# Kernel tuning notes

Measured on AMD Instinct MI355X. Metric: run time of the kernel, lower is better.

## Reference

```python
import jax, jax.numpy as jnp
import numpy as np

D, K = 128, 32
B, H, W = 32, 96, 96


def setup_inputs() -> dict:
    key = jax.random.key(0)
    k1, k2, k3 = jax.random.split(key, 3)
    X = jax.random.normal(k1, (B, D, H, W), dtype=jnp.float32)
    std1 = 1.0 / float(np.sqrt(K * D))
    codewords = jax.random.uniform(k2, (K, D), dtype=jnp.float32, minval=-std1, maxval=std1)
    scale = jax.random.uniform(k3, (K,), dtype=jnp.float32, minval=-1.0, maxval=0.0)
    return {"X": X, "codewords": codewords, "scale": scale}


def reference(X, codewords, scale):
    b, d = X.shape[0], X.shape[1]
    # [B, D, H, W] -> [B, N, D]
    Xf = X.reshape(b, d, -1).transpose(0, 2, 1)
    # scale_l2: SL[b,n,k] = scale_k^2 * ||x_bn - c_k||^2 (no (B,N,K,D) materialization)
    x2 = jnp.sum(Xf * Xf, axis=-1)                      # [B, N]
    c2 = jnp.sum(codewords * codewords, axis=-1)        # [K]
    xc = jnp.einsum('bnd,kd->bnk', Xf, codewords)       # [B, N, K]
    sl = (scale * scale)[None, None, :] * (x2[:, :, None] - 2.0 * xc + c2[None, None, :])
    A = jax.nn.softmax(sl, axis=2)                      # [B, N, K]
    # aggregate: E[b,k,d] = sum_n A[b,n,k] * (x[b,n,d] - c[k,d])
    E = jnp.einsum('bnk,bnd->bkd', A, Xf) - jnp.sum(A, axis=1)[:, :, None] * codewords[None, :, :]
    return E
```

## Files before the change

kernel.cpp:

```cpp
#include <hip/hip_runtime.h>

#define B_ 32
#define D_ 128
#define K_ 32
#define N_ 9216
#define NT 256
#define NS 64
#define XDN_S 72
#define AKN_S 72
#define X2S_S 68

typedef __bf16 bf16x8_t __attribute__((ext_vector_type(8)));
typedef float f32x4_t __attribute__((ext_vector_type(4)));

__device__ __forceinline__ unsigned short f2bf(float f) {
    unsigned u = __float_as_uint(f);
    u = (u + 0x7fffu + ((u >> 16) & 1u)) >> 16;
    return (unsigned short)u;
}
__device__ __forceinline__ unsigned f2bf_pk(float lo, float hi) {
    unsigned a = __float_as_uint(lo);
    a = (a + 0x7fffu + ((a >> 16) & 1u)) >> 16;
    unsigned b = __float_as_uint(hi);
    b = (b + 0x7fffu + ((b >> 16) & 1u)) & 0xffff0000u;
    return a | b;
}
__device__ __forceinline__ void bar_lds() {
    asm volatile("s_waitcnt lgkmcnt(0)\n\ts_barrier" ::: "memory");
}

__global__ __launch_bounds__(256, 3) void k_fused(
        const float* __restrict__ X, const float* __restrict__ cw,
        const float* __restrict__ scale, float* __restrict__ ws) {
    __shared__ __align__(16) unsigned short X_nd[NS * 128];
    __shared__ __align__(16) unsigned short X_dn[D_ * XDN_S];
    __shared__ __align__(16) unsigned short CWb[K_ * 128];
    __shared__ __align__(16) unsigned short Akn[K_ * AKN_S];
    __shared__ float x2s[16 * X2S_S];
    __shared__ float u_s[K_], w_s[K_];
    __shared__ float sAw[4 * 34];
    __shared__ float sA[K_];

    const int t = threadIdx.x;
    const int w = t >> 6;
    const int l = t & 63;
    const int lm = l & 15;
    const int lq = l >> 4;
    const int d8 = t >> 4;
    const int n4 = t & 15;
    const int b = blockIdx.x / 36;
    const int n0 = (blockIdx.x % 36) * NT;

    #pragma unroll
    for (int i = 0; i < 4; ++i) {
        int idx = t + 256 * i;
        int k = idx >> 5, d4 = idx & 31;
        float4 c = ((const float4*)cw)[idx];
        int phys = (d4 >> 1) ^ (k & 15);
        unsigned* p = (unsigned*)&CWb[k * 128 + phys * 8 + (d4 & 1) * 4];
        p[0] = f2bf_pk(c.x, c.y);
        p[1] = f2bf_pk(c.z, c.w);
    }
    if (t < 32) {
        float sc = scale[t];
        float s2 = sc * sc;
        const float4* cr = (const float4*)(cw + t * 128);
        float c2 = 0.f;
        #pragma unroll 8
        for (int i = 0; i < 32; ++i) {
            float4 v = cr[i];
            c2 += v.x * v.x + v.y * v.y + v.z * v.z + v.w * v.w;
        }
        u_s[t] = s2;
        w_s[t] = s2 * c2;
    }
    __syncthreads();
    const float u0 = u_s[lm], u1 = u_s[16 + lm];
    const float w0 = w_s[lm], w1 = w_s[16 + lm];

    f32x4_t acc2[2][2];
    #pragma unroll
    for (int a = 0; a < 2; ++a)
        #pragma unroll
        for (int c = 0; c < 2; ++c)
            acc2[a][c] = (f32x4_t){0.f, 0.f, 0.f, 0.f};
    float ps0 = 0.f, ps1 = 0.f;

    const float* Xg = X + ((size_t)b * D_ + d8 * 8) * N_ + n0 + n4 * 4;
    float4 v[8];
    #pragma unroll
    for (int j = 0; j < 8; ++j) v[j] = *(const float4*)(Xg + (size_t)j * N_);

    for (int s = 0; s < 4; ++s) {
        bar_lds();
        float4 vn[8];
        if (s < 3) {
            const float* Xg2 = Xg + (s + 1) * NS;
            #pragma unroll
            for (int j = 0; j < 8; ++j) vn[j] = *(const float4*)(Xg2 + (size_t)j * N_);
        }
        #pragma unroll
        for (int jn = 0; jn < 4; ++jn) {
            float a = 0.f;
            #pragma unroll
            for (int j = 0; j < 8; ++j) {
                float xv = (&v[j].x)[jn];
                a += xv * xv;
            }
            x2s[d8 * X2S_S + n4 * 4 + jn] = a;
        }
        #pragma unroll
        for (int j = 0; j < 8; ++j) {
            unsigned* p = (unsigned*)&X_dn[(d8 * 8 + j) * XDN_S + n4 * 4];
            p[0] = f2bf_pk(v[j].x, v[j].y);
            p[1] = f2bf_pk(v[j].z, v[j].w);
        }
        #pragma unroll
        for (int jn = 0; jn < 4; ++jn) {
            unsigned q[4];
            #pragma unroll
            for (int j2 = 0; j2 < 4; ++j2)
                q[j2] = f2bf_pk((&v[2 * j2].x)[jn], (&v[2 * j2 + 1].x)[jn]);
            int row = n4 * 4 + jn;
            *(uint4*)&X_nd[row * 128 + ((d8 ^ (row & 15)) * 8)] = *(const uint4*)q;
        }
        bar_lds();
        float x2row = 0.f;
        #pragma unroll
        for (int g = 0; g < 16; ++g) x2row += x2s[g * X2S_S + l];
        f32x4_t acc1[2];
        acc1[0] = (f32x4_t){0.f, 0.f, 0.f, 0.f};
        acc1[1] = (f32x4_t){0.f, 0.f, 0.f, 0.f};
        #pragma unroll
        for (int ks = 0; ks < 4; ++ks) {
            int g = (ks * 4 + lq) ^ lm;
            bf16x8_t a  = *(const bf16x8_t*)&X_nd[(w * 16 + lm) * 128 + g * 8];
            bf16x8_t b0 = *(const bf16x8_t*)&CWb[lm * 128 + g * 8];
            bf16x8_t b1 = *(const bf16x8_t*)&CWb[(16 + lm) * 128 + g * 8];
            acc1[0] = __builtin_amdgcn_mfma_f32_16x16x32_bf16(a, b0, acc1[0], 0, 0, 0);
            acc1[1] = __builtin_amdgcn_mfma_f32_16x16x32_bf16(a, b1, acc1[1], 0, 0, 0);
        }
        #pragma unroll
        for (int r = 0; r < 4; ++r) {
            int nl = w * 16 + lq * 4 + r;
            float x2v = __shfl(x2row, lq * 4 + r + w * 16 - w * 16);
            x2v = __shfl(x2row, lq * 4 + r);
            x2v = __shfl(x2row, nl);
            float sl0 = u0 * x2v + w0 - 2.f * u0 * acc1[0][r];
            float sl1 = u1 * x2v + w1 - 2.f * u1 * acc1[1][r];
            float m = fmaxf(sl0, sl1);
            m = fmaxf(m, __shfl_xor(m, 1));
            m = fmaxf(m, __shfl_xor(m, 2));
            m = fmaxf(m, __shfl_xor(m, 4));
            m = fmaxf(m, __shfl_xor(m, 8));
            float p0 = __expf(sl0 - m);
            float p1 = __expf(sl1 - m);
            float sum = p0 + p1;
            sum += __shfl_xor(sum, 1);
            sum += __shfl_xor(sum, 2);
            sum += __shfl_xor(sum, 4);
            sum += __shfl_xor(sum, 8);
            float inv = 1.f / sum;
            p0 *= inv; p1 *= inv;
            ps0 += p0; ps1 += p1;
            Akn[lm * AKN_S + nl] = f2bf(p0);
            Akn[(16 + lm) * AKN_S + nl] = f2bf(p1);
        }
        bar_lds();
        #pragma unroll
        for (int ks = 0; ks < 2; ++ks) {
            bf16x8_t xa0 = *(const bf16x8_t*)&X_dn[(w * 16 + lm) * XDN_S + ks * 32 + lq * 8];
            bf16x8_t xa1 = *(const bf16x8_t*)&X_dn[((w + 4) * 16 + lm) * XDN_S + ks * 32 + lq * 8];
            bf16x8_t pb0 = *(const bf16x8_t*)&Akn[lm * AKN_S + ks * 32 + lq * 8];
            bf16x8_t pb1 = *(const bf16x8_t*)&Akn[(16 + lm) * AKN_S + ks * 32 + lq * 8];
            acc2[0][0] = __builtin_amdgcn_mfma_f32_16x16x32_bf16(xa0, pb0, acc2[0][0], 0, 0, 0);
            acc2[0][1] = __builtin_amdgcn_mfma_f32_16x16x32_bf16(xa0, pb1, acc2[0][1], 0, 0, 0);
            acc2[1][0] = __builtin_amdgcn_mfma_f32_16x16x32_bf16(xa1, pb0, acc2[1][0], 0, 0, 0);
            acc2[1][1] = __builtin_amdgcn_mfma_f32_16x16x32_bf16(xa1, pb1, acc2[1][1], 0, 0, 0);
        }
        if (s < 3) {
            #pragma unroll
            for (int j = 0; j < 8; ++j) v[j] = vn[j];
        }
    }

    ps0 += __shfl_xor(ps0, 16); ps0 += __shfl_xor(ps0, 32);
    ps1 += __shfl_xor(ps1, 16); ps1 += __shfl_xor(ps1, 32);
    __syncthreads();
    if (l < 16) {
        sAw[w * 34 + l] = ps0;
        sAw[w * 34 + 16 + l] = ps1;
    }
    __syncthreads();
    if (t < 32) sA[t] = sAw[t] + sAw[34 + t] + sAw[68 + t] + sAw[102 + t];
    __syncthreads();

    float* pout = ws + (size_t)blockIdx.x * (K_ * D_);
    #pragma unroll
    for (int di = 0; di < 2; ++di) {
        #pragma unroll
        for (int kt = 0; kt < 2; ++kt) {
            const int d0 = (w + di * 4) * 16 + lq * 4;
            const int k  = kt * 16 + lm;
            float4 o;
            #pragma unroll
            for (int r = 0; r < 4; ++r)
                (&o.x)[r] = acc2[di][kt][r] - sA[k] * cw[k * 128 + d0 + r];
            *(float4*)&pout[k * 128 + d0] = o;
        }
    }
}

__global__ __launch_bounds__(256) void k_reduce(
        const float* __restrict__ ws, float* __restrict__ out) {
    int i = blockIdx.x * 256 + threadIdx.x;
    int b = i >> 10;
    int j = i & 1023;
    const float4* p = (const float4*)ws + (size_t)b * 36 * 1024 + j;
    float4 s = make_float4(0.f, 0.f, 0.f, 0.f);
    #pragma unroll
    for (int c = 0; c < 36; ++c) {
        float4 v = p[(size_t)c * 1024];
        s.x += v.x; s.y += v.y; s.z += v.z; s.w += v.w;
    }
    ((float4*)out)[i] = s;
}

extern "C" void kernel_launch(void* const* d_in, const int* in_sizes, int n_in,
                              void* d_out, int out_size, void* d_ws, size_t ws_size,
                              hipStream_t stream) {
    const float* X     = (const float*)d_in[0];
    const float* cw    = (const float*)d_in[1];
    const float* scale = (const float*)d_in[2];
    float* out = (float*)d_out;
    float* ws  = (float*)d_ws;

    k_fused <<<dim3(B_ * 36), dim3(256), 0, stream>>>(X, cw, scale, ws);
    k_reduce<<<dim3(128),     dim3(256), 0, stream>>>(ws, out);
}
```

Baseline: 226.2 us.

## Transpose first MFMA so softmax reduces in-lane, enlarge per-block chunk, use exp2

Swaps the operands of the first MFMA so each lane holds the 8 codeword logits of a single point. The softmax max and sum then reduce mostly within registers plus two cross-lane shuffles, instead of four-step butterflies repeated for every row. The log2(e) factor is folded into the scale so the exponential can use the native exp2 and rcp builtins. Each block now processes 384 points (6 stages) over 24 chunks, which cuts partial-sum traffic and the reduce kernel's work but leaves 768 blocks. The bf16 conversion uses the compiler cast, and the x2 partial store is vectorised.

```diff
diff --git a/kernel.cpp b/kernel.cpp
--- a/kernel.cpp
+++ b/kernel.cpp
@@ -4,26 +4,23 @@
 #define D_ 128
 #define K_ 32
 #define N_ 9216
-#define NT 256
+#define NT 384
+#define NCH 24
 #define NS 64
 #define XDN_S 72
 #define AKN_S 72
 #define X2S_S 68
+#define L2E 1.4426950408889634f
 
 typedef __bf16 bf16x8_t __attribute__((ext_vector_type(8)));
 typedef float f32x4_t __attribute__((ext_vector_type(4)));
 
 __device__ __forceinline__ unsigned short f2bf(float f) {
-    unsigned u = __float_as_uint(f);
-    u = (u + 0x7fffu + ((u >> 16) & 1u)) >> 16;
-    return (unsigned short)u;
+    return __builtin_bit_cast(unsigned short, (__bf16)f);
 }
 __device__ __forceinline__ unsigned f2bf_pk(float lo, float hi) {
-    unsigned a = __float_as_uint(lo);
-    a = (a + 0x7fffu + ((a >> 16) & 1u)) >> 16;
-    unsigned b = __float_as_uint(hi);
-    b = (b + 0x7fffu + ((b >> 16) & 1u)) & 0xffff0000u;
-    return a | b;
+    return (unsigned)__builtin_bit_cast(unsigned short, (__bf16)lo) |
+           ((unsigned)__builtin_bit_cast(unsigned short, (__bf16)hi) << 16);
 }
 __device__ __forceinline__ void bar_lds() {
     asm volatile("s_waitcnt lgkmcnt(0)\n\ts_barrier" ::: "memory");
@@ -48,8 +45,8 @@
     const int lq = l >> 4;
     const int d8 = t >> 4;
     const int n4 = t & 15;
-    const int b = blockIdx.x / 36;
-    const int n0 = (blockIdx.x % 36) * NT;
+    const int b = blockIdx.x / NCH;
+    const int n0 = (blockIdx.x % NCH) * NT;
 
     #pragma unroll
     for (int i = 0; i < 4; ++i) {
@@ -63,7 +60,7 @@
     }
     if (t < 32) {
         float sc = scale[t];
-        float s2 = sc * sc;
+        float s2 = sc * sc * L2E;
         const float4* cr = (const float4*)(cw + t * 128);
         float c2 = 0.f;
         #pragma unroll 8
@@ -75,8 +72,12 @@
         w_s[t] = s2 * c2;
     }
     __syncthreads();
-    const float u0 = u_s[lm], u1 = u_s[16 + lm];
-    const float w0 = w_s[lm], w1 = w_s[16 + lm];
+    float uk[8], wk[8];
+    #pragma unroll
+    for (int r = 0; r < 4; ++r) {
+        uk[r]     = u_s[lq * 4 + r];      wk[r]     = w_s[lq * 4 + r];
+        uk[4 + r] = u_s[16 + lq * 4 + r]; wk[4 + r] = w_s[16 + lq * 4 + r];
+    }
 
     f32x4_t acc2[2][2];
     #pragma unroll
@@ -84,30 +85,36 @@
         #pragma unroll
         for (int c = 0; c < 2; ++c)
             acc2[a][c] = (f32x4_t){0.f, 0.f, 0.f, 0.f};
-    float ps0 = 0.f, ps1 = 0.f;
+    float ps[8];
+    #pragma unroll
+    for (int r = 0; r < 8; ++r) ps[r] = 0.f;
 
     const float* Xg = X + ((size_t)b * D_ + d8 * 8) * N_ + n0 + n4 * 4;
     float4 v[8];
     #pragma unroll
     for (int j = 0; j < 8; ++j) v[j] = *(const float4*)(Xg + (size_t)j * N_);
 
-    for (int s = 0; s < 4; ++s) {
+    for (int s = 0; s < 6; ++s) {
         bar_lds();
         float4 vn[8];
-        if (s < 3) {
+        if (s < 5) {
             const float* Xg2 = Xg + (s + 1) * NS;
             #pragma unroll
             for (int j = 0; j < 8; ++j) vn[j] = *(const float4*)(Xg2 + (size_t)j * N_);
         }
-        #pragma unroll
-        for (int jn = 0; jn < 4; ++jn) {
-            float a = 0.f;
-            #pragma unroll
-            for (int j = 0; j < 8; ++j) {
-                float xv = (&v[j].x)[jn];
-                a += xv * xv;
+        {
+            float a4[4];
+            #pragma unroll
+            for (int jn = 0; jn < 4; ++jn) {
+                float a = 0.f;
+                #pragma unroll
+                for (int j = 0; j < 8; ++j) {
+                    float xv = (&v[j].x)[jn];
+                    a += xv * xv;
+                }
+                a4[jn] = a;
             }
-            x2s[d8 * X2S_S + n4 * 4 + jn] = a;
+            *(float4*)&x2s[d8 * X2S_S + n4 * 4] = make_float4(a4[0], a4[1], a4[2], a4[3]);
         }
         #pragma unroll
         for (int j = 0; j < 8; ++j) {
@@ -125,46 +132,47 @@
             *(uint4*)&X_nd[row * 128 + ((d8 ^ (row & 15)) * 8)] = *(const uint4*)q;
         }
         bar_lds();
-        float x2row = 0.f;
-        #pragma unroll
-        for (int g = 0; g < 16; ++g) x2row += x2s[g * X2S_S + l];
+        float x2v = 0.f;
+        #pragma unroll
+        for (int g = 0; g < 16; ++g) x2v += x2s[g * X2S_S + w * 16 + lm];
         f32x4_t acc1[2];
         acc1[0] = (f32x4_t){0.f, 0.f, 0.f, 0.f};
         acc1[1] = (f32x4_t){0.f, 0.f, 0.f, 0.f};
         #pragma unroll
         for (int ks = 0; ks < 4; ++ks) {
             int g = (ks * 4 + lq) ^ lm;
-            bf16x8_t a  = *(const bf16x8_t*)&X_nd[(w * 16 + lm) * 128 + g * 8];
-            bf16x8_t b0 = *(const bf16x8_t*)&CWb[lm * 128 + g * 8];
-            bf16x8_t b1 = *(const bf16x8_t*)&CWb[(16 + lm) * 128 + g * 8];
-            acc1[0] = __builtin_amdgcn_mfma_f32_16x16x32_bf16(a, b0, acc1[0], 0, 0, 0);
-            acc1[1] = __builtin_amdgcn_mfma_f32_16x16x32_bf16(a, b1, acc1[1], 0, 0, 0);
-        }
+            bf16x8_t xb = *(const bf16x8_t*)&X_nd[(w * 16 + lm) * 128 + g * 8];
+            bf16x8_t c0 = *(const bf16x8_t*)&CWb[lm * 128 + g * 8];
+            bf16x8_t c1 = *(const bf16x8_t*)&CWb[(16 + lm) * 128 + g * 8];
+            acc1[0] = __builtin_amdgcn_mfma_f32_16x16x32_bf16(c0, xb, acc1[0], 0, 0, 0);
+            acc1[1] = __builtin_amdgcn_mfma_f32_16x16x32_bf16(c1, xb, acc1[1], 0, 0, 0);
+        }
+        float sl[8];
         #pragma unroll
         for (int r = 0; r < 4; ++r) {
-            int nl = w * 16 + lq * 4 + r;
-            float x2v = __shfl(x2row, lq * 4 + r + w * 16 - w * 16);
-            x2v = __shfl(x2row, lq * 4 + r);
-            x2v = __shfl(x2row, nl);
-            float sl0 = u0 * x2v + w0 - 2.f * u0 * acc1[0][r];
-            float sl1 = u1 * x2v + w1 - 2.f * u1 * acc1[1][r];
-            float m = fmaxf(sl0, sl1);
-            m = fmaxf(m, __shfl_xor(m, 1));
-            m = fmaxf(m, __shfl_xor(m, 2));
-            m = fmaxf(m, __shfl_xor(m, 4));
-            m = fmaxf(m, __shfl_xor(m, 8));
-            float p0 = __expf(sl0 - m);
-            float p1 = __expf(sl1 - m);
-            float sum = p0 + p1;
-            sum += __shfl_xor(sum, 1);
-            sum += __shfl_xor(sum, 2);
-            sum += __shfl_xor(sum, 4);
-            sum += __shfl_xor(sum, 8);
-            float inv = 1.f / sum;
-            p0 *= inv; p1 *= inv;
-            ps0 += p0; ps1 += p1;
-            Akn[lm * AKN_S + nl] = f2bf(p0);
-            Akn[(16 + lm) * AKN_S + nl] = f2bf(p1);
+            sl[r]     = fmaf(uk[r],     fmaf(acc1[0][r], -2.f, x2v), wk[r]);
+            sl[4 + r] = fmaf(uk[4 + r], fmaf(acc1[1][r], -2.f, x2v), wk[4 + r]);
+        }
+        float m = fmaxf(fmaxf(fmaxf(sl[0], sl[1]), fmaxf(sl[2], sl[3])),
+                        fmaxf(fmaxf(sl[4], sl[5]), fmaxf(sl[6], sl[7])));
+        m = fmaxf(m, __shfl_xor(m, 16));
+        m = fmaxf(m, __shfl_xor(m, 32));
+        float p[8], sum = 0.f;
+        #pragma unroll
+        for (int r = 0; r < 8; ++r) {
+            p[r] = __builtin_amdgcn_exp2f(sl[r] - m);
+            sum += p[r];
+        }
+        sum += __shfl_xor(sum, 16);
+        sum += __shfl_xor(sum, 32);
+        float inv = __builtin_amdgcn_rcpf(sum);
+        const int nl = w * 16 + lm;
+        #pragma unroll
+        for (int r = 0; r < 4; ++r) {
+            float p0 = p[r] * inv, p1 = p[4 + r] * inv;
+            ps[r] += p0; ps[4 + r] += p1;
+            Akn[(lq * 4 + r) * AKN_S + nl]        = f2bf(p0);
+            Akn[(16 + lq * 4 + r) * AKN_S + nl]   = f2bf(p1);
         }
         bar_lds();
         #pragma unroll
@@ -178,18 +186,26 @@
             acc2[1][0] = __builtin_amdgcn_mfma_f32_16x16x32_bf16(xa1, pb0, acc2[1][0], 0, 0, 0);
             acc2[1][1] = __builtin_amdgcn_mfma_f32_16x16x32_bf16(xa1, pb1, acc2[1][1], 0, 0, 0);
         }
-        if (s < 3) {
+        if (s < 5) {
             #pragma unroll
             for (int j = 0; j < 8; ++j) v[j] = vn[j];
         }
     }
 
-    ps0 += __shfl_xor(ps0, 16); ps0 += __shfl_xor(ps0, 32);
-    ps1 += __shfl_xor(ps1, 16); ps1 += __shfl_xor(ps1, 32);
-    __syncthreads();
-    if (l < 16) {
-        sAw[w * 34 + l] = ps0;
-        sAw[w * 34 + 16 + l] = ps1;
+    #pragma unroll
+    for (int r = 0; r < 8; ++r) {
+        ps[r] += __shfl_xor(ps[r], 1);
+        ps[r] += __shfl_xor(ps[r], 2);
+        ps[r] += __shfl_xor(ps[r], 4);
+        ps[r] += __shfl_xor(ps[r], 8);
+    }
+    __syncthreads();
+    if (lm == 0) {
+        #pragma unroll
+        for (int r = 0; r < 4; ++r) {
+            sAw[w * 34 + lq * 4 + r]      = ps[r];
+            sAw[w * 34 + 16 + lq * 4 + r] = ps[4 + r];
+        }
     }
     __syncthreads();
     if (t < 32) sA[t] = sAw[t] + sAw[34 + t] + sAw[68 + t] + sAw[102 + t];
@@ -216,10 +232,10 @@
     int i = blockIdx.x * 256 + threadIdx.x;
     int b = i >> 10;
     int j = i & 1023;
-    const float4* p = (const float4*)ws + (size_t)b * 36 * 1024 + j;
+    const float4* p = (const float4*)ws + (size_t)b * NCH * 1024 + j;
     float4 s = make_float4(0.f, 0.f, 0.f, 0.f);
     #pragma unroll
-    for (int c = 0; c < 36; ++c) {
+    for (int c = 0; c < NCH; ++c) {
         float4 v = p[(size_t)c * 1024];
         s.x += v.x; s.y += v.y; s.z += v.z; s.w += v.w;
     }
@@ -235,6 +251,6 @@
     float* out = (float*)d_out;
     float* ws  = (float*)d_ws;
 
-    k_fused <<<dim3(B_ * 36), dim3(256), 0, stream>>>(X, cw, scale, ws);
-    k_reduce<<<dim3(128),     dim3(256), 0, stream>>>(ws, out);
-}
+    k_fused <<<dim3(B_ * NCH), dim3(256), 0, stream>>>(X, cw, scale, ws);
+    k_reduce<<<dim3(128),      dim3(256), 0, stream>>>(ws, out);
+}
```

Result: no change. 226.3 us (+0.0%).
